# Optimization experiments

Measured on AMD Instinct MI355X. Metric: run time of the kernel, lower is better.

## Reference

```python
import jax, jax.numpy as jnp
import numpy as np

DIM = 256
HEAD_DIM = 32
HEADS = DIM // HEAD_DIM
SHAPE = (64, 64)          # (H, W) patch grid
WS = 8                    # window size
SHIFT = 4                 # shift size (ws // 2)
SCALE = HEAD_DIM ** -0.5
WS2 = WS * WS


def _rel_indices(ws):
    # relative position index for every (query, key) pair in a window
    a = np.arange(ws)
    y1, x1, y2, x2 = np.meshgrid(a, a, a, a, indexing='ij')
    idx = (y1 - y2 + ws - 1) * (2 * ws - 1) + (x1 - x2 + ws - 1)
    return idx.reshape(ws * ws, ws * ws)  # (ws2, ws2)


def _shift_mask(shape, ws, shift):
    # region labels per patch, 9 regions from the 3x3 slice grid
    H, W = shape
    region = np.zeros((H, W), dtype=np.int32)
    slices = [slice(0, -ws), slice(-ws, -shift), slice(-shift, None)]
    num = 0
    for i in slices:
        for j in slices:
            region[i, j] = num
            num += 1
    # window-partition the region map -> (n_windows, ws2)
    nH, nW = H // ws, W // ws
    r = region.reshape(nH, ws, nW, ws).transpose(0, 2, 1, 3).reshape(nH * nW, ws * ws)
    # True where query and key come from different regions
    return (r[:, None, :] - r[:, :, None]) != 0  # (nw, ws2, ws2)


REL_IDX = jnp.asarray(_rel_indices(WS))                 # (ws2, ws2) int
MASK = jnp.asarray(_shift_mask(SHAPE, WS, SHIFT))       # (nw, ws2, ws2) bool


def _split_windows(x, ws):
    # (b, H, W, C) -> (b * nH * nW, ws*ws, C)
    b, H, W, C = x.shape
    x = x.reshape(b, H // ws, ws, W // ws, ws, C)
    x = x.transpose(0, 1, 3, 2, 4, 5)
    return x.reshape(-1, ws * ws, C)


def _merge_windows(x, shape, ws):
    # inverse of _split_windows
    H, W = shape
    nH, nW = H // ws, W // ws
    C = x.shape[-1]
    x = x.reshape(-1, nH, nW, ws, ws, C)
    x = x.transpose(0, 1, 3, 2, 4, 5)
    return x.reshape(-1, H, W, C)


def setup_inputs() -> dict:
    key = jax.random.key(0)
    ks = jax.random.split(key, 6)
    s = 0.02
    return {
        'x': jax.random.normal(ks[0], (32, SHAPE[0] * SHAPE[1], DIM), jnp.float32),
        'w_qkv': jax.random.normal(ks[1], (3 * DIM, DIM), jnp.float32) * s,
        'b_qkv': jax.random.normal(ks[2], (3 * DIM,), jnp.float32) * s,
        'w_out': jax.random.normal(ks[3], (DIM, DIM), jnp.float32) * s,
        'b_out': jax.random.normal(ks[4], (DIM,), jnp.float32) * s,
        'pos_enc': jax.random.normal(ks[5], (HEADS, (2 * WS - 1) ** 2), jnp.float32) * s,
    }


def reference(x, w_qkv, b_qkv, w_out, b_out, pos_enc):
    B, N, C = x.shape
    H, W = SHAPE
    nw = (H // WS) * (W // WS)

    xg = x.reshape(B, H, W, C)
    if SHIFT > 0:
        xg = jnp.roll(xg, (-SHIFT, -SHIFT), axis=(1, 2))
    xw = _split_windows(xg, WS)                        # (B*nw, ws2, C)

    qkv = xw @ w_qkv.T + b_qkv                         # (B*nw, ws2, 3C)
    qkv = qkv.reshape(-1, WS2, 3, HEADS, HEAD_DIM)
    q, k, v = (qkv[:, :, i].transpose(0, 2, 1, 3) for i in range(3))  # (Bn, h, ws2, hd)

    attn = jnp.einsum('bhqd,bhkd->bhqk', q, k) * SCALE  # (Bn, h, ws2, ws2)
    bias = pos_enc[:, REL_IDX]                          # (h, ws2, ws2)
    attn = attn + bias[None]

    if SHIFT > 0:
        attn = attn.reshape(B, nw, HEADS, WS2, WS2)
        attn = jnp.where(MASK[None, :, None], -jnp.inf, attn)
        attn = attn.reshape(B * nw, HEADS, WS2, WS2)

    attn = jax.nn.softmax(attn, axis=-1)
    out = jnp.einsum('bhqk,bhkd->bhqd', attn, v)        # (Bn, h, ws2, hd)
    out = out.transpose(0, 2, 1, 3).reshape(-1, WS2, C)
    out = out @ w_out.T + b_out                         # (Bn, ws2, C)

    out = _merge_windows(out, SHAPE, WS)                # (B, H, W, C)
    if SHIFT > 0:
        out = jnp.roll(out, (SHIFT, SHIFT), axis=(1, 2))
    return out.reshape(B, N, C)
```

## Files before the change

kernel.cpp:

```cpp
#include <hip/hip_runtime.h>
#include <stdint.h>


typedef short short8 __attribute__((ext_vector_type(8)));
typedef short s16x4 __attribute__((ext_vector_type(4)));
typedef float f32x4 __attribute__((ext_vector_type(4)));

typedef __attribute__((address_space(1))) uint32_t g_u32;
typedef __attribute__((address_space(3))) uint32_t l_u32;

#define SCALE 0.17677669529663687f

__device__ __forceinline__ uint16_t f2bf(float f) {
  union { float f; uint32_t u; } c; c.f = f;
  uint32_t r = c.u + 0x7FFFu + ((c.u >> 16) & 1u);
  return (uint16_t)(r >> 16);
}

__device__ __forceinline__ void g2lds16(const void* g, void* l) {
  __builtin_amdgcn_global_load_lds((const g_u32*)g, (l_u32*)l, 16, 0, 0);
}

__global__ __launch_bounds__(256) void cvtw_kernel(const float* __restrict__ wq,
                                                   const float* __restrict__ wo,
                                                   uint16_t* __restrict__ out) {
  int i = (blockIdx.x * 256 + threadIdx.x) * 8;
  const float* src = (i < 196608) ? (wq + i) : (wo + (i - 196608));
  f32x4 a = *(const f32x4*)src;
  f32x4 b = *(const f32x4*)(src + 4);
  short8 v;
  v[0] = (short)f2bf(a[0]); v[1] = (short)f2bf(a[1]);
  v[2] = (short)f2bf(a[2]); v[3] = (short)f2bf(a[3]);
  v[4] = (short)f2bf(b[0]); v[5] = (short)f2bf(b[1]);
  v[6] = (short)f2bf(b[2]); v[7] = (short)f2bf(b[3]);
  *(short8*)(out + i) = v;
}

__global__ __launch_bounds__(256) void bias_kernel(const float* __restrict__ pe,
                                                   float* __restrict__ bm) {
  int bx = blockIdx.x;
  int wd = bx >> 3, head = bx & 7;
  int hw = wd >> 3, ww = wd & 7;
  int tid = threadIdx.x;
  int kk = tid >> 2, a0 = (tid & 3) * 4;
  int jy = kk >> 3, jx = kk & 7;
  int hj = hw * 8 + jy, xj = ww * 8 + jx;
  int rj = (hj >= 60 ? 2 : (hj >= 56 ? 1 : 0)) * 3 + (xj >= 60 ? 2 : (xj >= 56 ? 1 : 0));
  float* dst = bm + (size_t)bx * 4096 + kk * 64 + a0 * 4;
  for (int aa = 0; aa < 4; ++aa) {
    int a = a0 + aa;
    f32x4 v;
#pragma unroll
    for (int ni = 0; ni < 4; ++ni) {
      int i = ni * 16 + a;
      int iy = i >> 3, ix = i & 7;
      int hi = hw * 8 + iy, xi = ww * 8 + ix;
      int ri = (hi >= 60 ? 2 : (hi >= 56 ? 1 : 0)) * 3 + (xi >= 60 ? 2 : (xi >= 56 ? 1 : 0));
      v[ni] = (ri != rj) ? -1e30f : pe[head * 225 + (iy - jy + 7) * 15 + (ix - jx + 7)];
    }
    *(f32x4*)(dst + aa * 4) = v;
  }
}

__global__ __launch_bounds__(256, 2) void wattn_kernel(
    const float* __restrict__ x, const uint16_t* __restrict__ wq,
    const float* __restrict__ bqkv, const float* __restrict__ bm,
    uint16_t* __restrict__ ao) {
  __shared__ uint16_t sm[40960];
  uint16_t* As = sm;
  const int tid = threadIdx.x, lane = tid & 63, wv = tid >> 6;
  const int quad = lane >> 4, l15 = lane & 15;
  const int b = blockIdx.x;
  const int w = ((b >> 4) << 3) + (b & 7);
  const int hh = (b >> 3) & 1;
  const int h = hh * 4 + wv;
  const int wd = w & 63, bb = w >> 6;
  f32x4 zero = {0.f, 0.f, 0.f, 0.f};

  {
    const int rl = tid >> 3;
    const int cg = tid & 7;
#pragma unroll
    for (int pass = 0; pass < 2; ++pass) {
      int row = pass * 32 + rl;
      int hy = (wd >> 3) * 8 + (row >> 3);
      int xx = (wd & 7) * 8 + (row & 7);
      const float* sp = x + (size_t)(bb * 4096 + (((hy + 4) & 63) << 6) + ((xx + 4) & 63)) * 256;
      int psw = (row >> 1) & 3;
#pragma unroll
      for (int j = 0; j < 4; ++j) {
        int c0 = cg * 8 + j * 64;
        f32x4 a = *(const f32x4*)(sp + c0);
        f32x4 d = *(const f32x4*)(sp + c0 + 4);
        short8 v;
        v[0] = (short)f2bf(a[0]); v[1] = (short)f2bf(a[1]);
        v[2] = (short)f2bf(a[2]); v[3] = (short)f2bf(a[3]);
        v[4] = (short)f2bf(d[0]); v[5] = (short)f2bf(d[1]);
        v[6] = (short)f2bf(d[2]); v[7] = (short)f2bf(d[3]);
        int ks = c0 >> 5, g = (c0 >> 3) & 3;
        *(short8*)&As[(ks * 64 + row) * 32 + ((g ^ psw) << 3)] = v;
      }
    }
  }

  const int fsw = (quad ^ ((l15 >> 1) & 3)) << 3;
  uint16_t* qk = sm + 16384 + wv * 6144;

  const uint16_t* bb0 = wq + (size_t)(h * 32 + l15) * 256 + quad * 8;

  short8 bfr[2][6];
#pragma unroll
  for (int ni = 0; ni < 6; ++ni)
    bfr[0][ni] = *(const short8*)(bb0 + (ni >> 1) * 65536 + (ni & 1) * 4096);

  f32x4 acc[4][6];
#pragma unroll
  for (int mi = 0; mi < 4; ++mi)
#pragma unroll
    for (int ni = 0; ni < 6; ++ni) acc[mi][ni] = zero;

  __syncthreads();

#pragma unroll
  for (int ks = 0; ks < 8; ++ks) {
    const int cur = ks & 1;
    if (ks < 7) {
#pragma unroll
      for (int ni = 0; ni < 6; ++ni)
        bfr[cur ^ 1][ni] = *(const short8*)(bb0 + (ni >> 1) * 65536 + (ni & 1) * 4096 + (ks + 1) * 32);
    }
    short8 af[4];
#pragma unroll
    for (int mi = 0; mi < 4; ++mi)
      af[mi] = *(const short8*)&As[(ks * 64 + mi * 16 + l15) * 32 + fsw];
#pragma unroll
    for (int mi = 0; mi < 4; ++mi)
#pragma unroll
      for (int ni = 0; ni < 6; ++ni)
        acc[mi][ni] = __builtin_amdgcn_mfma_f32_16x16x32_bf16(af[mi], bfr[cur][ni], acc[mi][ni], 0, 0, 0);
  }

  float bqv[6];
#pragma unroll
  for (int ni = 0; ni < 6; ++ni)
    bqv[ni] = bqkv[(ni >> 1) * 256 + h * 32 + (ni & 1) * 16 + l15];

#pragma unroll
  for (int ni = 0; ni < 4; ++ni) {
    uint16_t* dst = qk + (ni >> 1) * 2048;
    int d = (ni & 1) * 16 + l15, dg = d >> 3;
#pragma unroll
    for (int mi = 0; mi < 4; ++mi)
#pragma unroll
      for (int r = 0; r < 4; ++r) {
        int t = mi * 16 + quad * 4 + r;
        dst[t * 32 + (((dg ^ ((t >> 1) & 3)) << 3) | (d & 7))] =
            f2bf(acc[mi][ni][r] + bqv[ni]);
      }
  }
  {
    uint16_t* vdst = qk + 4096;
#pragma unroll
    for (int ni = 4; ni < 6; ++ni) {
      int d = (ni - 4) * 16 + l15;
#pragma unroll
      for (int mi = 0; mi < 4; ++mi) {
        int t0 = mi * 16 + quad * 4;
        s16x4 pv;
        pv[0] = (short)f2bf(acc[mi][ni][0] + bqv[ni]);
        pv[1] = (short)f2bf(acc[mi][ni][1] + bqv[ni]);
        pv[2] = (short)f2bf(acc[mi][ni][2] + bqv[ni]);
        pv[3] = (short)f2bf(acc[mi][ni][3] + bqv[ni]);
        *(s16x4*)&vdst[d * 64 + (t0 ^ ((d & 7) << 3))] = pv;
      }
    }
  }

  __syncthreads();

  const uint16_t* qb2 = qk;
  const uint16_t* kb2 = qk + 2048;
  const uint16_t* vb2 = qk + 4096;
  const float* bmh = bm + ((size_t)wd * 8 + h) * 4096;

  short8 ak[4], bq[4];
#pragma unroll
  for (int mi = 0; mi < 4; ++mi)
    ak[mi] = *(const short8*)&kb2[(mi * 16 + l15) * 32 + fsw];
#pragma unroll
  for (int ni = 0; ni < 4; ++ni)
    bq[ni] = *(const short8*)&qb2[(ni * 16 + l15) * 32 + fsw];

  f32x4 s[4][4];
#pragma unroll
  for (int mi = 0; mi < 4; ++mi)
#pragma unroll
    for (int ni = 0; ni < 4; ++ni)
      s[mi][ni] = __builtin_amdgcn_mfma_f32_16x16x32_bf16(ak[mi], bq[ni], zero, 0, 0, 0);

#pragma unroll
  for (int mi = 0; mi < 4; ++mi)
#pragma unroll
    for (int r = 0; r < 4; ++r) {
      int kk = mi * 16 + quad * 4 + r;
      f32x4 b4 = *(const f32x4*)&bmh[kk * 64 + l15 * 4];
#pragma unroll
      for (int ni = 0; ni < 4; ++ni)
        s[mi][ni][r] = s[mi][ni][r] * SCALE + b4[ni];
    }

#pragma unroll
  for (int ni = 0; ni < 4; ++ni) {
    float mx = s[0][ni][0];
#pragma unroll
    for (int mi = 0; mi < 4; ++mi)
#pragma unroll
      for (int r = 0; r < 4; ++r) mx = fmaxf(mx, s[mi][ni][r]);
    mx = fmaxf(mx, __shfl_xor(mx, 16, 64));
    mx = fmaxf(mx, __shfl_xor(mx, 32, 64));
    float sum = 0.f;
#pragma unroll
    for (int mi = 0; mi < 4; ++mi)
#pragma unroll
      for (int r = 0; r < 4; ++r) {
        float e = __expf(s[mi][ni][r] - mx);
        s[mi][ni][r] = e;
        sum += e;
      }
    sum += __shfl_xor(sum, 16, 64);
    sum += __shfl_xor(sum, 32, 64);
    float inv = 1.f / sum;
#pragma unroll
    for (int mi = 0; mi < 4; ++mi)
#pragma unroll
      for (int r = 0; r < 4; ++r) s[mi][ni][r] *= inv;
  }

  uint16_t* Pw = sm + wv * 4096;
#pragma unroll
  for (int mi = 0; mi < 4; ++mi)
#pragma unroll
    for (int ni = 0; ni < 4; ++ni)
#pragma unroll
      for (int rp = 0; rp < 2; ++rp) {
        int kk = mi * 16 + quad * 4 + rp * 2;
        int q = ni * 16 + l15;
        uint32_t pk = (uint32_t)f2bf(s[mi][ni][rp * 2]) |
                      ((uint32_t)f2bf(s[mi][ni][rp * 2 + 1]) << 16);
        *(uint32_t*)&Pw[q * 64 + ((((kk >> 3) ^ (q & 7)) << 3) | (kk & 7))] = pk;
      }

  f32x4 o[4][2];
#pragma unroll
  for (int mi = 0; mi < 4; ++mi) { o[mi][0] = zero; o[mi][1] = zero; }
#pragma unroll
  for (int ki = 0; ki < 2; ++ki) {
    int tc = ki * 32 + quad * 8;
    short8 vf0 = *(const short8*)&vb2[l15 * 64 + (tc ^ ((l15 & 7) << 3))];
    short8 vf1 = *(const short8*)&vb2[(16 + l15) * 64 + (tc ^ ((l15 & 7) << 3))];
#pragma unroll
    for (int mi = 0; mi < 4; ++mi) {
      int q = mi * 16 + l15;
      short8 pa = *(const short8*)&Pw[q * 64 + (((ki * 4 + quad) ^ (q & 7)) << 3)];
      o[mi][0] = __builtin_amdgcn_mfma_f32_16x16x32_bf16(pa, vf0, o[mi][0], 0, 0, 0);
      o[mi][1] = __builtin_amdgcn_mfma_f32_16x16x32_bf16(pa, vf1, o[mi][1], 0, 0, 0);
    }
  }
#pragma unroll
  for (int mi = 0; mi < 4; ++mi)
#pragma unroll
    for (int ni = 0; ni < 2; ++ni)
#pragma unroll
      for (int r = 0; r < 4; ++r) {
        int t = mi * 16 + quad * 4 + r;
        ao[(size_t)(w * 64 + t) * 256 + h * 32 + ni * 16 + l15] = f2bf(o[mi][ni][r]);
      }
}

__global__ __launch_bounds__(256) void oproj_kernel(
    const uint16_t* __restrict__ aob, const uint16_t* __restrict__ wo,
    const float* __restrict__ bout, float* __restrict__ out) {
  __shared__ uint16_t sm[16384];
  uint16_t* As = sm;
  uint16_t* Bs = sm + 8192;
  const int tid = threadIdx.x, lane = tid & 63, wv = tid >> 6;
  const int quad = lane >> 4, l15 = lane & 15;
  const int n0 = blockIdx.x * 128;
  const int m0 = blockIdx.y * 128;

  const int c0 = wv * 2, c1 = c0 + 1;
  const int perm = ((lane & 3) ^ ((lane >> 3) & 3)) * 8;
  const int fsw = (quad ^ ((l15 >> 1) & 3)) * 8;
  const uint16_t* ap0 = aob + (size_t)(m0 + c0 * 16 + (lane >> 2)) * 256 + perm;
  const uint16_t* ap1 = aob + (size_t)(m0 + c1 * 16 + (lane >> 2)) * 256 + perm;
  const uint16_t* bp0 = wo + (size_t)(n0 + c0 * 16 + (lane >> 2)) * 256 + perm;
  const uint16_t* bp1 = wo + (size_t)(n0 + c1 * 16 + (lane >> 2)) * 256 + perm;

  const int wm = (wv & 1) * 64, wn = (wv >> 1) * 64;
  f32x4 zero = {0.f, 0.f, 0.f, 0.f};
  f32x4 acc[4][4];
#pragma unroll
  for (int mi = 0; mi < 4; ++mi)
#pragma unroll
    for (int ni = 0; ni < 4; ++ni) acc[mi][ni] = zero;

  g2lds16(ap0, &As[c0 * 512]);
  g2lds16(ap1, &As[c1 * 512]);
  g2lds16(bp0, &Bs[c0 * 512]);
  g2lds16(bp1, &Bs[c1 * 512]);

#pragma unroll
  for (int ks = 0; ks < 8; ++ks) {
    __syncthreads();
    if (ks < 7) {
      int nb = ((ks + 1) & 1) * 4096, k0 = (ks + 1) * 32;
      g2lds16(ap0 + k0, &As[nb + c0 * 512]);
      g2lds16(ap1 + k0, &As[nb + c1 * 512]);
      g2lds16(bp0 + k0, &Bs[nb + c0 * 512]);
      g2lds16(bp1 + k0, &Bs[nb + c1 * 512]);
    }
    int buf = (ks & 1) * 4096;
    short8 af[4], bf[4];
#pragma unroll
    for (int mi = 0; mi < 4; ++mi)
      af[mi] = *(const short8*)&As[buf + (wm + mi * 16 + l15) * 32 + fsw];
#pragma unroll
    for (int ni = 0; ni < 4; ++ni)
      bf[ni] = *(const short8*)&Bs[buf + (wn + ni * 16 + l15) * 32 + fsw];
#pragma unroll
    for (int mi = 0; mi < 4; ++mi)
#pragma unroll
      for (int ni = 0; ni < 4; ++ni)
        acc[mi][ni] = __builtin_amdgcn_mfma_f32_16x16x32_bf16(af[mi], bf[ni], acc[mi][ni], 0, 0, 0);
  }

  float bo4[4];
#pragma unroll
  for (int ni = 0; ni < 4; ++ni) bo4[ni] = bout[n0 + wn + ni * 16 + l15];
#pragma unroll
  for (int mi = 0; mi < 4; ++mi) {
    int mb = m0 + wm + mi * 16 + quad * 4;
    int w = mb >> 6, t0 = mb & 63;
    int b = w >> 6, wd = w & 63;
    int hw2 = wd >> 3, ww2 = wd & 7;
#pragma unroll
    for (int r = 0; r < 4; ++r) {
      int t = t0 + r;
      int h = hw2 * 8 + (t >> 3), xx = ww2 * 8 + (t & 7);
      int row = (((h + 4) & 63) << 6) | ((xx + 4) & 63);
      float* op = out + ((size_t)b * 4096 + row) * 256 + n0 + wn;
#pragma unroll
      for (int ni = 0; ni < 4; ++ni) op[ni * 16 + l15] = acc[mi][ni][r] + bo4[ni];
    }
  }
}

extern "C" void kernel_launch(void* const* d_in, const int* in_sizes, int n_in,
                              void* d_out, int out_size, void* d_ws, size_t ws_size,
                              hipStream_t stream) {
  const float* x = (const float*)d_in[0];
  const float* w_qkv = (const float*)d_in[1];
  const float* b_qkv = (const float*)d_in[2];
  const float* w_out = (const float*)d_in[3];
  const float* b_out = (const float*)d_in[4];
  const float* pos_enc = (const float*)d_in[5];
  float* out = (float*)d_out;

  uint8_t* ws = (uint8_t*)d_ws;
  uint16_t* aob = (uint16_t*)(ws);
  uint16_t* wqb = (uint16_t*)(ws + 67108864);
  uint16_t* wob = (uint16_t*)(ws + 67502080);
  float*    bmt = (float*)   (ws + 67633152);

  cvtw_kernel<<<128, 256, 0, stream>>>(w_qkv, w_out, wqb);
  bias_kernel<<<512, 256, 0, stream>>>(pos_enc, bmt);
  wattn_kernel<<<4096, 256, 0, stream>>>(x, wqb, b_qkv, bmt, aob);
  oproj_kernel<<<dim3(2, 1024), 256, 0, stream>>>(aob, wob, b_out, out);
}
```

Baseline: 367.7 us.

## Fuse output projection into window-attention kernel with one block per window

Merges the attention kernel and the separate output-projection GEMM into one kernel. Each 512-thread block now handles one window with all eight heads (one wave per head), stages the per-head attention output in LDS in bf16, and runs the output projection from LDS with weights streamed from global memory. This removes the bf16 intermediate round trip through global memory and one launch. The trade-offs are higher LDS use (128KB per block), a block-wide barrier, and a P matrix staged in two halves to fit.

```diff
diff --git a/kernel.cpp b/kernel.cpp
--- a/kernel.cpp
+++ b/kernel.cpp
@@ -5,9 +5,6 @@
 typedef short short8 __attribute__((ext_vector_type(8)));
 typedef short s16x4 __attribute__((ext_vector_type(4)));
 typedef float f32x4 __attribute__((ext_vector_type(4)));
-
-typedef __attribute__((address_space(1))) uint32_t g_u32;
-typedef __attribute__((address_space(3))) uint32_t l_u32;
 
 #define SCALE 0.17677669529663687f
 
@@ -15,10 +12,6 @@
   union { float f; uint32_t u; } c; c.f = f;
   uint32_t r = c.u + 0x7FFFu + ((c.u >> 16) & 1u);
   return (uint16_t)(r >> 16);
-}
-
-__device__ __forceinline__ void g2lds16(const void* g, void* l) {
-  __builtin_amdgcn_global_load_lds((const g_u32*)g, (l_u32*)l, 16, 0, 0);
 }
 
 __global__ __launch_bounds__(256) void cvtw_kernel(const float* __restrict__ wq,
@@ -62,44 +55,39 @@
   }
 }
 
-__global__ __launch_bounds__(256, 2) void wattn_kernel(
+__global__ __launch_bounds__(512, 2) void swattn_kernel(
     const float* __restrict__ x, const uint16_t* __restrict__ wq,
-    const float* __restrict__ bqkv, const float* __restrict__ bm,
-    uint16_t* __restrict__ ao) {
-  __shared__ uint16_t sm[40960];
+    const uint16_t* __restrict__ wo, const float* __restrict__ bqkv,
+    const float* __restrict__ bout, const float* __restrict__ bm,
+    float* __restrict__ out) {
+  __shared__ uint16_t sm[65536];
   uint16_t* As = sm;
   const int tid = threadIdx.x, lane = tid & 63, wv = tid >> 6;
   const int quad = lane >> 4, l15 = lane & 15;
-  const int b = blockIdx.x;
-  const int w = ((b >> 4) << 3) + (b & 7);
-  const int hh = (b >> 3) & 1;
-  const int h = hh * 4 + wv;
+  const int w = blockIdx.x;
+  const int h = wv;
   const int wd = w & 63, bb = w >> 6;
   f32x4 zero = {0.f, 0.f, 0.f, 0.f};
 
   {
-    const int rl = tid >> 3;
+    const int row = tid >> 3;
     const int cg = tid & 7;
-#pragma unroll
-    for (int pass = 0; pass < 2; ++pass) {
-      int row = pass * 32 + rl;
-      int hy = (wd >> 3) * 8 + (row >> 3);
-      int xx = (wd & 7) * 8 + (row & 7);
-      const float* sp = x + (size_t)(bb * 4096 + (((hy + 4) & 63) << 6) + ((xx + 4) & 63)) * 256;
-      int psw = (row >> 1) & 3;
-#pragma unroll
-      for (int j = 0; j < 4; ++j) {
-        int c0 = cg * 8 + j * 64;
-        f32x4 a = *(const f32x4*)(sp + c0);
-        f32x4 d = *(const f32x4*)(sp + c0 + 4);
-        short8 v;
-        v[0] = (short)f2bf(a[0]); v[1] = (short)f2bf(a[1]);
-        v[2] = (short)f2bf(a[2]); v[3] = (short)f2bf(a[3]);
-        v[4] = (short)f2bf(d[0]); v[5] = (short)f2bf(d[1]);
-        v[6] = (short)f2bf(d[2]); v[7] = (short)f2bf(d[3]);
-        int ks = c0 >> 5, g = (c0 >> 3) & 3;
-        *(short8*)&As[(ks * 64 + row) * 32 + ((g ^ psw) << 3)] = v;
-      }
+    int hy = (wd >> 3) * 8 + (row >> 3);
+    int xx = (wd & 7) * 8 + (row & 7);
+    const float* sp = x + (size_t)(bb * 4096 + (((hy + 4) & 63) << 6) + ((xx + 4) & 63)) * 256;
+    int psw = (row >> 1) & 3;
+#pragma unroll
+    for (int j = 0; j < 4; ++j) {
+      int c0 = cg * 8 + j * 64;
+      f32x4 a = *(const f32x4*)(sp + c0);
+      f32x4 d = *(const f32x4*)(sp + c0 + 4);
+      short8 v;
+      v[0] = (short)f2bf(a[0]); v[1] = (short)f2bf(a[1]);
+      v[2] = (short)f2bf(a[2]); v[3] = (short)f2bf(a[3]);
+      v[4] = (short)f2bf(d[0]); v[5] = (short)f2bf(d[1]);
+      v[6] = (short)f2bf(d[2]); v[7] = (short)f2bf(d[3]);
+      int ks = c0 >> 5, g = (c0 >> 3) & 3;
+      *(short8*)&As[(ks * 64 + row) * 32 + ((g ^ psw) << 3)] = v;
     }
   }
 
@@ -236,121 +224,102 @@
       for (int r = 0; r < 4; ++r) s[mi][ni][r] *= inv;
   }
 
-  uint16_t* Pw = sm + wv * 4096;
-#pragma unroll
-  for (int mi = 0; mi < 4; ++mi)
-#pragma unroll
-    for (int ni = 0; ni < 4; ++ni)
-#pragma unroll
-      for (int rp = 0; rp < 2; ++rp) {
-        int kk = mi * 16 + quad * 4 + rp * 2;
-        int q = ni * 16 + l15;
-        uint32_t pk = (uint32_t)f2bf(s[mi][ni][rp * 2]) |
-                      ((uint32_t)f2bf(s[mi][ni][rp * 2 + 1]) << 16);
-        *(uint32_t*)&Pw[q * 64 + ((((kk >> 3) ^ (q & 7)) << 3) | (kk & 7))] = pk;
-      }
-
+  uint16_t* Pw = sm + wv * 2048;
   f32x4 o[4][2];
 #pragma unroll
   for (int mi = 0; mi < 4; ++mi) { o[mi][0] = zero; o[mi][1] = zero; }
 #pragma unroll
-  for (int ki = 0; ki < 2; ++ki) {
-    int tc = ki * 32 + quad * 8;
-    short8 vf0 = *(const short8*)&vb2[l15 * 64 + (tc ^ ((l15 & 7) << 3))];
-    short8 vf1 = *(const short8*)&vb2[(16 + l15) * 64 + (tc ^ ((l15 & 7) << 3))];
-#pragma unroll
-    for (int mi = 0; mi < 4; ++mi) {
-      int q = mi * 16 + l15;
-      short8 pa = *(const short8*)&Pw[q * 64 + (((ki * 4 + quad) ^ (q & 7)) << 3)];
-      o[mi][0] = __builtin_amdgcn_mfma_f32_16x16x32_bf16(pa, vf0, o[mi][0], 0, 0, 0);
-      o[mi][1] = __builtin_amdgcn_mfma_f32_16x16x32_bf16(pa, vf1, o[mi][1], 0, 0, 0);
-    }
-  }
-#pragma unroll
-  for (int mi = 0; mi < 4; ++mi)
-#pragma unroll
-    for (int ni = 0; ni < 2; ++ni)
-#pragma unroll
-      for (int r = 0; r < 4; ++r) {
-        int t = mi * 16 + quad * 4 + r;
-        ao[(size_t)(w * 64 + t) * 256 + h * 32 + ni * 16 + l15] = f2bf(o[mi][ni][r]);
-      }
-}
-
-__global__ __launch_bounds__(256) void oproj_kernel(
-    const uint16_t* __restrict__ aob, const uint16_t* __restrict__ wo,
-    const float* __restrict__ bout, float* __restrict__ out) {
-  __shared__ uint16_t sm[16384];
-  uint16_t* As = sm;
-  uint16_t* Bs = sm + 8192;
-  const int tid = threadIdx.x, lane = tid & 63, wv = tid >> 6;
-  const int quad = lane >> 4, l15 = lane & 15;
-  const int n0 = blockIdx.x * 128;
-  const int m0 = blockIdx.y * 128;
-
-  const int c0 = wv * 2, c1 = c0 + 1;
-  const int perm = ((lane & 3) ^ ((lane >> 3) & 3)) * 8;
-  const int fsw = (quad ^ ((l15 >> 1) & 3)) * 8;
-  const uint16_t* ap0 = aob + (size_t)(m0 + c0 * 16 + (lane >> 2)) * 256 + perm;
-  const uint16_t* ap1 = aob + (size_t)(m0 + c1 * 16 + (lane >> 2)) * 256 + perm;
-  const uint16_t* bp0 = wo + (size_t)(n0 + c0 * 16 + (lane >> 2)) * 256 + perm;
-  const uint16_t* bp1 = wo + (size_t)(n0 + c1 * 16 + (lane >> 2)) * 256 + perm;
-
-  const int wm = (wv & 1) * 64, wn = (wv >> 1) * 64;
-  f32x4 zero = {0.f, 0.f, 0.f, 0.f};
-  f32x4 acc[4][4];
-#pragma unroll
-  for (int mi = 0; mi < 4; ++mi)
-#pragma unroll
-    for (int ni = 0; ni < 4; ++ni) acc[mi][ni] = zero;
-
-  g2lds16(ap0, &As[c0 * 512]);
-  g2lds16(ap1, &As[c1 * 512]);
-  g2lds16(bp0, &Bs[c0 * 512]);
-  g2lds16(bp1, &Bs[c1 * 512]);
+  for (int p = 0; p < 2; ++p) {
+#pragma unroll
+    for (int mi = 0; mi < 4; ++mi)
+#pragma unroll
+      for (int nn = 0; nn < 2; ++nn) {
+        int ni = 2 * p + nn;
+        int qp = nn * 16 + l15;
+#pragma unroll
+        for (int rp = 0; rp < 2; ++rp) {
+          int kk = mi * 16 + quad * 4 + rp * 2;
+          uint32_t pk = (uint32_t)f2bf(s[mi][ni][rp * 2]) |
+                        ((uint32_t)f2bf(s[mi][ni][rp * 2 + 1]) << 16);
+          *(uint32_t*)&Pw[qp * 64 + ((((kk >> 3) ^ (qp & 7)) << 3) | (kk & 7))] = pk;
+        }
+      }
+#pragma unroll
+    for (int ki = 0; ki < 2; ++ki) {
+      int tc = ki * 32 + quad * 8;
+      short8 vf0 = *(const short8*)&vb2[l15 * 64 + (tc ^ ((l15 & 7) << 3))];
+      short8 vf1 = *(const short8*)&vb2[(16 + l15) * 64 + (tc ^ ((l15 & 7) << 3))];
+#pragma unroll
+      for (int mi2 = 0; mi2 < 2; ++mi2) {
+        int mi = 2 * p + mi2;
+        int qp = mi2 * 16 + l15;
+        short8 pa = *(const short8*)&Pw[qp * 64 + (((ki * 4 + quad) ^ (qp & 7)) << 3)];
+        o[mi][0] = __builtin_amdgcn_mfma_f32_16x16x32_bf16(pa, vf0, o[mi][0], 0, 0, 0);
+        o[mi][1] = __builtin_amdgcn_mfma_f32_16x16x32_bf16(pa, vf1, o[mi][1], 0, 0, 0);
+      }
+    }
+  }
+
+  {
+    uint16_t* aodst = qk;
+#pragma unroll
+    for (int ni = 0; ni < 2; ++ni) {
+      int d = ni * 16 + l15, dg = d >> 3;
+#pragma unroll
+      for (int mi = 0; mi < 4; ++mi)
+#pragma unroll
+        for (int r = 0; r < 4; ++r) {
+          int t = mi * 16 + quad * 4 + r;
+          aodst[t * 32 + (((dg ^ ((t >> 1) & 3)) << 3) | (d & 7))] = f2bf(o[mi][ni][r]);
+        }
+    }
+  }
+
+  __syncthreads();
+
+  const uint16_t* bbase2 = wo + (size_t)(wv * 32 + l15) * 256 + quad * 8;
+  short8 bfr2[2][2];
+#pragma unroll
+  for (int ni = 0; ni < 2; ++ni)
+    bfr2[0][ni] = *(const short8*)(bbase2 + ni * 4096);
+
+  f32x4 acc2[4][2];
+#pragma unroll
+  for (int mi = 0; mi < 4; ++mi) { acc2[mi][0] = zero; acc2[mi][1] = zero; }
 
 #pragma unroll
   for (int ks = 0; ks < 8; ++ks) {
-    __syncthreads();
+    const int cur = ks & 1;
     if (ks < 7) {
-      int nb = ((ks + 1) & 1) * 4096, k0 = (ks + 1) * 32;
-      g2lds16(ap0 + k0, &As[nb + c0 * 512]);
-      g2lds16(ap1 + k0, &As[nb + c1 * 512]);
-      g2lds16(bp0 + k0, &Bs[nb + c0 * 512]);
-      g2lds16(bp1 + k0, &Bs[nb + c1 * 512]);
-    }
-    int buf = (ks & 1) * 4096;
-    short8 af[4], bf[4];
-#pragma unroll
-    for (int mi = 0; mi < 4; ++mi)
-      af[mi] = *(const short8*)&As[buf + (wm + mi * 16 + l15) * 32 + fsw];
-#pragma unroll
-    for (int ni = 0; ni < 4; ++ni)
-      bf[ni] = *(const short8*)&Bs[buf + (wn + ni * 16 + l15) * 32 + fsw];
-#pragma unroll
-    for (int mi = 0; mi < 4; ++mi)
-#pragma unroll
-      for (int ni = 0; ni < 4; ++ni)
-        acc[mi][ni] = __builtin_amdgcn_mfma_f32_16x16x32_bf16(af[mi], bf[ni], acc[mi][ni], 0, 0, 0);
-  }
-
-  float bo4[4];
-#pragma unroll
-  for (int ni = 0; ni < 4; ++ni) bo4[ni] = bout[n0 + wn + ni * 16 + l15];
+#pragma unroll
+      for (int ni = 0; ni < 2; ++ni)
+        bfr2[cur ^ 1][ni] = *(const short8*)(bbase2 + ni * 4096 + (ks + 1) * 32);
+    }
+    short8 af2[4];
+#pragma unroll
+    for (int mi = 0; mi < 4; ++mi)
+      af2[mi] = *(const short8*)&sm[16384 + ks * 6144 + (mi * 16 + l15) * 32 + fsw];
+#pragma unroll
+    for (int mi = 0; mi < 4; ++mi)
+#pragma unroll
+      for (int ni = 0; ni < 2; ++ni)
+        acc2[mi][ni] = __builtin_amdgcn_mfma_f32_16x16x32_bf16(af2[mi], bfr2[cur][ni], acc2[mi][ni], 0, 0, 0);
+  }
+
+  float bo4[2];
+#pragma unroll
+  for (int ni = 0; ni < 2; ++ni) bo4[ni] = bout[wv * 32 + ni * 16 + l15];
+  const int hw2 = wd >> 3, ww2 = wd & 7;
 #pragma unroll
   for (int mi = 0; mi < 4; ++mi) {
-    int mb = m0 + wm + mi * 16 + quad * 4;
-    int w = mb >> 6, t0 = mb & 63;
-    int b = w >> 6, wd = w & 63;
-    int hw2 = wd >> 3, ww2 = wd & 7;
 #pragma unroll
     for (int r = 0; r < 4; ++r) {
-      int t = t0 + r;
-      int h = hw2 * 8 + (t >> 3), xx = ww2 * 8 + (t & 7);
-      int row = (((h + 4) & 63) << 6) | ((xx + 4) & 63);
-      float* op = out + ((size_t)b * 4096 + row) * 256 + n0 + wn;
-#pragma unroll
-      for (int ni = 0; ni < 4; ++ni) op[ni * 16 + l15] = acc[mi][ni][r] + bo4[ni];
+      int t = mi * 16 + quad * 4 + r;
+      int hy = hw2 * 8 + (t >> 3), xx = ww2 * 8 + (t & 7);
+      int row = (((hy + 4) & 63) << 6) | ((xx + 4) & 63);
+      float* op = out + ((size_t)bb * 4096 + row) * 256 + wv * 32;
+#pragma unroll
+      for (int ni = 0; ni < 2; ++ni) op[ni * 16 + l15] = acc2[mi][ni][r] + bo4[ni];
     }
   }
 }
@@ -367,13 +336,11 @@
   float* out = (float*)d_out;
 
   uint8_t* ws = (uint8_t*)d_ws;
-  uint16_t* aob = (uint16_t*)(ws);
-  uint16_t* wqb = (uint16_t*)(ws + 67108864);
-  uint16_t* wob = (uint16_t*)(ws + 67502080);
-  float*    bmt = (float*)   (ws + 67633152);
+  uint16_t* wqb = (uint16_t*)(ws);
+  uint16_t* wob = (uint16_t*)(ws + 393216);
+  float*    bmt = (float*)   (ws + 524288);
 
   cvtw_kernel<<<128, 256, 0, stream>>>(w_qkv, w_out, wqb);
   bias_kernel<<<512, 256, 0, stream>>>(pos_enc, bmt);
-  wattn_kernel<<<4096, 256, 0, stream>>>(x, wqb, b_qkv, bmt, aob);
-  oproj_kernel<<<dim3(2, 1024), 256, 0, stream>>>(aob, wob, b_out, out);
-}
+  swattn_kernel<<<2048, 512, 0, stream>>>(x, wqb, wob, b_qkv, b_out, bmt, out);
+}
```

Result: slower. 407.7 us (+10.9%).

## Shrink window-attention LDS footprint to fit three blocks per CU

Applied to the files above, without the earlier changes.

Cuts the wattn kernel's shared memory from 80KB to 48KB so three blocks can share a CU, and raises the launch-bounds occupancy hint to 3. To fit, the X tile is staged in two K-halves with an extra barrier. Q is written late into the freed A region, and the softmax probabilities are written and consumed in two 32-query halves that reuse the Q buffer. The gain in latency hiding from more resident blocks is traded for extra syncs, serialized P staging, and tighter register limits that may cause spills.

```diff
diff --git a/kernel.cpp b/kernel.cpp
--- a/kernel.cpp
+++ b/kernel.cpp
@@ -62,11 +62,11 @@
   }
 }
 
-__global__ __launch_bounds__(256, 2) void wattn_kernel(
+__global__ __launch_bounds__(256, 3) void wattn_kernel(
     const float* __restrict__ x, const uint16_t* __restrict__ wq,
     const float* __restrict__ bqkv, const float* __restrict__ bm,
     uint16_t* __restrict__ ao) {
-  __shared__ uint16_t sm[40960];
+  __shared__ uint16_t sm[24576];
   uint16_t* As = sm;
   const int tid = threadIdx.x, lane = tid & 63, wv = tid >> 6;
   const int quad = lane >> 4, l15 = lane & 15;
@@ -77,37 +77,16 @@
   const int wd = w & 63, bb = w >> 6;
   f32x4 zero = {0.f, 0.f, 0.f, 0.f};
 
+  const int srow = tid >> 2, scg = tid & 3;
+  const float* sp;
   {
-    const int rl = tid >> 3;
-    const int cg = tid & 7;
-#pragma unroll
-    for (int pass = 0; pass < 2; ++pass) {
-      int row = pass * 32 + rl;
-      int hy = (wd >> 3) * 8 + (row >> 3);
-      int xx = (wd & 7) * 8 + (row & 7);
-      const float* sp = x + (size_t)(bb * 4096 + (((hy + 4) & 63) << 6) + ((xx + 4) & 63)) * 256;
-      int psw = (row >> 1) & 3;
-#pragma unroll
-      for (int j = 0; j < 4; ++j) {
-        int c0 = cg * 8 + j * 64;
-        f32x4 a = *(const f32x4*)(sp + c0);
-        f32x4 d = *(const f32x4*)(sp + c0 + 4);
-        short8 v;
-        v[0] = (short)f2bf(a[0]); v[1] = (short)f2bf(a[1]);
-        v[2] = (short)f2bf(a[2]); v[3] = (short)f2bf(a[3]);
-        v[4] = (short)f2bf(d[0]); v[5] = (short)f2bf(d[1]);
-        v[6] = (short)f2bf(d[2]); v[7] = (short)f2bf(d[3]);
-        int ks = c0 >> 5, g = (c0 >> 3) & 3;
-        *(short8*)&As[(ks * 64 + row) * 32 + ((g ^ psw) << 3)] = v;
-      }
-    }
-  }
-
-  const int fsw = (quad ^ ((l15 >> 1) & 3)) << 3;
-  uint16_t* qk = sm + 16384 + wv * 6144;
+    int hy = (wd >> 3) * 8 + (srow >> 3);
+    int xx = (wd & 7) * 8 + (srow & 7);
+    sp = x + (size_t)(bb * 4096 + (((hy + 4) & 63) << 6) + ((xx + 4) & 63)) * 256;
+  }
+  const int spsw = (srow >> 1) & 3;
 
   const uint16_t* bb0 = wq + (size_t)(h * 32 + l15) * 256 + quad * 8;
-
   short8 bfr[2][6];
 #pragma unroll
   for (int ni = 0; ni < 6; ++ni)
@@ -119,47 +98,63 @@
 #pragma unroll
     for (int ni = 0; ni < 6; ++ni) acc[mi][ni] = zero;
 
-  __syncthreads();
-
-#pragma unroll
-  for (int ks = 0; ks < 8; ++ks) {
-    const int cur = ks & 1;
-    if (ks < 7) {
-#pragma unroll
-      for (int ni = 0; ni < 6; ++ni)
-        bfr[cur ^ 1][ni] = *(const short8*)(bb0 + (ni >> 1) * 65536 + (ni & 1) * 4096 + (ks + 1) * 32);
-    }
-    short8 af[4];
-#pragma unroll
-    for (int mi = 0; mi < 4; ++mi)
-      af[mi] = *(const short8*)&As[(ks * 64 + mi * 16 + l15) * 32 + fsw];
-#pragma unroll
-    for (int mi = 0; mi < 4; ++mi)
-#pragma unroll
-      for (int ni = 0; ni < 6; ++ni)
-        acc[mi][ni] = __builtin_amdgcn_mfma_f32_16x16x32_bf16(af[mi], bfr[cur][ni], acc[mi][ni], 0, 0, 0);
-  }
-
+  const int fsw = (quad ^ ((l15 >> 1) & 3)) << 3;
+
+  for (int hf = 0; hf < 2; ++hf) {
+    if (hf) __syncthreads();
+#pragma unroll
+    for (int j = 0; j < 4; ++j) {
+      int c0 = scg * 8 + j * 32;
+      const float* p = sp + hf * 128 + c0;
+      f32x4 a = *(const f32x4*)p;
+      f32x4 d = *(const f32x4*)(p + 4);
+      short8 v;
+      v[0] = (short)f2bf(a[0]); v[1] = (short)f2bf(a[1]);
+      v[2] = (short)f2bf(a[2]); v[3] = (short)f2bf(a[3]);
+      v[4] = (short)f2bf(d[0]); v[5] = (short)f2bf(d[1]);
+      v[6] = (short)f2bf(d[2]); v[7] = (short)f2bf(d[3]);
+      *(short8*)&As[(j * 64 + srow) * 32 + ((scg ^ spsw) << 3)] = v;
+    }
+    __syncthreads();
+#pragma unroll
+    for (int ksl = 0; ksl < 4; ++ksl) {
+      const int ks = hf * 4 + ksl;
+      const int cur = ks & 1;
+      if (ks < 7) {
+#pragma unroll
+        for (int ni = 0; ni < 6; ++ni)
+          bfr[cur ^ 1][ni] = *(const short8*)(bb0 + (ni >> 1) * 65536 + (ni & 1) * 4096 + (ks + 1) * 32);
+      }
+      short8 af[4];
+#pragma unroll
+      for (int mi = 0; mi < 4; ++mi)
+        af[mi] = *(const short8*)&As[(ksl * 64 + mi * 16 + l15) * 32 + fsw];
+#pragma unroll
+      for (int mi = 0; mi < 4; ++mi)
+#pragma unroll
+        for (int ni = 0; ni < 6; ++ni)
+          acc[mi][ni] = __builtin_amdgcn_mfma_f32_16x16x32_bf16(af[mi], bfr[cur][ni], acc[mi][ni], 0, 0, 0);
+    }
+  }
+
+  uint16_t* kvs = sm + 8192 + wv * 4096;
   float bqv[6];
 #pragma unroll
   for (int ni = 0; ni < 6; ++ni)
     bqv[ni] = bqkv[(ni >> 1) * 256 + h * 32 + (ni & 1) * 16 + l15];
 
 #pragma unroll
-  for (int ni = 0; ni < 4; ++ni) {
-    uint16_t* dst = qk + (ni >> 1) * 2048;
-    int d = (ni & 1) * 16 + l15, dg = d >> 3;
-#pragma unroll
-    for (int mi = 0; mi < 4; ++mi)
-#pragma unroll
-      for (int r = 0; r < 4; ++r) {
-        int t = mi * 16 + quad * 4 + r;
-        dst[t * 32 + (((dg ^ ((t >> 1) & 3)) << 3) | (d & 7))] =
-            f2bf(acc[mi][ni][r] + bqv[ni]);
-      }
+  for (int ni = 2; ni < 4; ++ni) {
+    int d = (ni & 1) * 16 + l15;
+    uint16_t* kd = kvs + quad * 4 * 32 + ((((d >> 3) ^ quad) << 3) | (d & 7));
+#pragma unroll
+    for (int mi = 0; mi < 4; ++mi)
+#pragma unroll
+      for (int r = 0; r < 4; ++r)
+        kd[mi * 512 + r * 32] = f2bf(acc[mi][ni][r] + bqv[ni]);
   }
   {
-    uint16_t* vdst = qk + 4096;
+    uint16_t* vdst = kvs + 2048;
 #pragma unroll
     for (int ni = 4; ni < 6; ++ni) {
       int d = (ni - 4) * 16 + l15;
@@ -178,19 +173,28 @@
 
   __syncthreads();
 
-  const uint16_t* qb2 = qk;
-  const uint16_t* kb2 = qk + 2048;
-  const uint16_t* vb2 = qk + 4096;
+  uint16_t* sq = sm + wv * 2048;
+#pragma unroll
+  for (int ni = 0; ni < 2; ++ni) {
+    int d = ni * 16 + l15;
+    uint16_t* qd = sq + quad * 4 * 32 + ((((d >> 3) ^ quad) << 3) | (d & 7));
+#pragma unroll
+    for (int mi = 0; mi < 4; ++mi)
+#pragma unroll
+      for (int r = 0; r < 4; ++r)
+        qd[mi * 512 + r * 32] = f2bf(acc[mi][ni][r] + bqv[ni]);
+  }
+
+  const int fsw2 = (quad ^ ((l15 >> 2) & 3)) << 3;
+  short8 bq[4], ak[4];
+#pragma unroll
+  for (int ni = 0; ni < 4; ++ni)
+    bq[ni] = *(const short8*)&sq[(ni * 16 + l15) * 32 + fsw2];
+#pragma unroll
+  for (int mi = 0; mi < 4; ++mi)
+    ak[mi] = *(const short8*)&kvs[(mi * 16 + l15) * 32 + fsw2];
+
   const float* bmh = bm + ((size_t)wd * 8 + h) * 4096;
-
-  short8 ak[4], bq[4];
-#pragma unroll
-  for (int mi = 0; mi < 4; ++mi)
-    ak[mi] = *(const short8*)&kb2[(mi * 16 + l15) * 32 + fsw];
-#pragma unroll
-  for (int ni = 0; ni < 4; ++ni)
-    bq[ni] = *(const short8*)&qb2[(ni * 16 + l15) * 32 + fsw];
-
   f32x4 s[4][4];
 #pragma unroll
   for (int mi = 0; mi < 4; ++mi)
@@ -236,36 +240,43 @@
       for (int r = 0; r < 4; ++r) s[mi][ni][r] *= inv;
   }
 
-  uint16_t* Pw = sm + wv * 4096;
-#pragma unroll
-  for (int mi = 0; mi < 4; ++mi)
-#pragma unroll
-    for (int ni = 0; ni < 4; ++ni)
-#pragma unroll
-      for (int rp = 0; rp < 2; ++rp) {
-        int kk = mi * 16 + quad * 4 + rp * 2;
-        int q = ni * 16 + l15;
-        uint32_t pk = (uint32_t)f2bf(s[mi][ni][rp * 2]) |
-                      ((uint32_t)f2bf(s[mi][ni][rp * 2 + 1]) << 16);
-        *(uint32_t*)&Pw[q * 64 + ((((kk >> 3) ^ (q & 7)) << 3) | (kk & 7))] = pk;
-      }
-
+  uint16_t* Pw = sq;
+  const uint16_t* vb2 = kvs + 2048;
   f32x4 o[4][2];
 #pragma unroll
   for (int mi = 0; mi < 4; ++mi) { o[mi][0] = zero; o[mi][1] = zero; }
 #pragma unroll
-  for (int ki = 0; ki < 2; ++ki) {
-    int tc = ki * 32 + quad * 8;
-    short8 vf0 = *(const short8*)&vb2[l15 * 64 + (tc ^ ((l15 & 7) << 3))];
-    short8 vf1 = *(const short8*)&vb2[(16 + l15) * 64 + (tc ^ ((l15 & 7) << 3))];
-#pragma unroll
-    for (int mi = 0; mi < 4; ++mi) {
-      int q = mi * 16 + l15;
-      short8 pa = *(const short8*)&Pw[q * 64 + (((ki * 4 + quad) ^ (q & 7)) << 3)];
-      o[mi][0] = __builtin_amdgcn_mfma_f32_16x16x32_bf16(pa, vf0, o[mi][0], 0, 0, 0);
-      o[mi][1] = __builtin_amdgcn_mfma_f32_16x16x32_bf16(pa, vf1, o[mi][1], 0, 0, 0);
-    }
-  }
+  for (int p = 0; p < 2; ++p) {
+#pragma unroll
+    for (int mi = 0; mi < 4; ++mi)
+#pragma unroll
+      for (int nn = 0; nn < 2; ++nn) {
+        int ni = 2 * p + nn;
+        int qp = nn * 16 + l15;
+#pragma unroll
+        for (int rp = 0; rp < 2; ++rp) {
+          int kk = mi * 16 + quad * 4 + rp * 2;
+          uint32_t pk = (uint32_t)f2bf(s[mi][ni][rp * 2]) |
+                        ((uint32_t)f2bf(s[mi][ni][rp * 2 + 1]) << 16);
+          *(uint32_t*)&Pw[qp * 64 + ((((kk >> 3) ^ (qp & 7)) << 3) | (kk & 7))] = pk;
+        }
+      }
+#pragma unroll
+    for (int ki = 0; ki < 2; ++ki) {
+      int tc = ki * 32 + quad * 8;
+      short8 vf0 = *(const short8*)&vb2[l15 * 64 + (tc ^ ((l15 & 7) << 3))];
+      short8 vf1 = *(const short8*)&vb2[(16 + l15) * 64 + (tc ^ ((l15 & 7) << 3))];
+#pragma unroll
+      for (int mi2 = 0; mi2 < 2; ++mi2) {
+        int mi = 2 * p + mi2;
+        int qp = mi2 * 16 + l15;
+        short8 pa = *(const short8*)&Pw[qp * 64 + (((ki * 4 + quad) ^ (qp & 7)) << 3)];
+        o[mi][0] = __builtin_amdgcn_mfma_f32_16x16x32_bf16(pa, vf0, o[mi][0], 0, 0, 0);
+        o[mi][1] = __builtin_amdgcn_mfma_f32_16x16x32_bf16(pa, vf1, o[mi][1], 0, 0, 0);
+      }
+    }
+  }
+
 #pragma unroll
   for (int mi = 0; mi < 4; ++mi)
 #pragma unroll
```

Result: no change. 371.1 us (+0.9%).

## Process all heads of a window per 512-thread block with aliased LDS buffers

Applied to the files above, without the earlier changes.

The window-attention kernel now launches one 512-thread block per window, with each of 8 waves handling one head. Previously two 256-thread blocks each took 4 heads, so each window's input tile was loaded from global memory and converted to bf16 twice; now it is done once. LDS use drops from 80 KB to 64 KB by reusing one per-wave region for Q, then K, then the probability matrix, which is written and consumed in two halves, with V kept separately. The smaller footprint aims to fit more resident waves per CU. The cost is tighter ordering of LDS reuse inside each wave and larger blocks.

```diff
diff --git a/kernel.cpp b/kernel.cpp
--- a/kernel.cpp
+++ b/kernel.cpp
@@ -62,52 +62,44 @@
   }
 }
 
-__global__ __launch_bounds__(256, 2) void wattn_kernel(
+__global__ __launch_bounds__(512, 4) void wattn_kernel(
     const float* __restrict__ x, const uint16_t* __restrict__ wq,
     const float* __restrict__ bqkv, const float* __restrict__ bm,
     uint16_t* __restrict__ ao) {
-  __shared__ uint16_t sm[40960];
+  __shared__ uint16_t sm[32768];
   uint16_t* As = sm;
   const int tid = threadIdx.x, lane = tid & 63, wv = tid >> 6;
   const int quad = lane >> 4, l15 = lane & 15;
-  const int b = blockIdx.x;
-  const int w = ((b >> 4) << 3) + (b & 7);
-  const int hh = (b >> 3) & 1;
-  const int h = hh * 4 + wv;
+  const int w = blockIdx.x;
+  const int h = wv;
   const int wd = w & 63, bb = w >> 6;
   f32x4 zero = {0.f, 0.f, 0.f, 0.f};
 
   {
-    const int rl = tid >> 3;
+    const int row = tid >> 3;
     const int cg = tid & 7;
-#pragma unroll
-    for (int pass = 0; pass < 2; ++pass) {
-      int row = pass * 32 + rl;
-      int hy = (wd >> 3) * 8 + (row >> 3);
-      int xx = (wd & 7) * 8 + (row & 7);
-      const float* sp = x + (size_t)(bb * 4096 + (((hy + 4) & 63) << 6) + ((xx + 4) & 63)) * 256;
-      int psw = (row >> 1) & 3;
-#pragma unroll
-      for (int j = 0; j < 4; ++j) {
-        int c0 = cg * 8 + j * 64;
-        f32x4 a = *(const f32x4*)(sp + c0);
-        f32x4 d = *(const f32x4*)(sp + c0 + 4);
-        short8 v;
-        v[0] = (short)f2bf(a[0]); v[1] = (short)f2bf(a[1]);
-        v[2] = (short)f2bf(a[2]); v[3] = (short)f2bf(a[3]);
-        v[4] = (short)f2bf(d[0]); v[5] = (short)f2bf(d[1]);
-        v[6] = (short)f2bf(d[2]); v[7] = (short)f2bf(d[3]);
-        int ks = c0 >> 5, g = (c0 >> 3) & 3;
-        *(short8*)&As[(ks * 64 + row) * 32 + ((g ^ psw) << 3)] = v;
-      }
+    int hy = (wd >> 3) * 8 + (row >> 3);
+    int xx = (wd & 7) * 8 + (row & 7);
+    const float* sp = x + (size_t)(bb * 4096 + (((hy + 4) & 63) << 6) + ((xx + 4) & 63)) * 256;
+    int psw = (row >> 1) & 3;
+#pragma unroll
+    for (int j = 0; j < 4; ++j) {
+      int c0 = cg * 8 + j * 64;
+      f32x4 a = *(const f32x4*)(sp + c0);
+      f32x4 d = *(const f32x4*)(sp + c0 + 4);
+      short8 v;
+      v[0] = (short)f2bf(a[0]); v[1] = (short)f2bf(a[1]);
+      v[2] = (short)f2bf(a[2]); v[3] = (short)f2bf(a[3]);
+      v[4] = (short)f2bf(d[0]); v[5] = (short)f2bf(d[1]);
+      v[6] = (short)f2bf(d[2]); v[7] = (short)f2bf(d[3]);
+      int ks = c0 >> 5, g = (c0 >> 3) & 3;
+      *(short8*)&As[(ks * 64 + row) * 32 + ((g ^ psw) << 3)] = v;
     }
   }
 
   const int fsw = (quad ^ ((l15 >> 1) & 3)) << 3;
-  uint16_t* qk = sm + 16384 + wv * 6144;
 
   const uint16_t* bb0 = wq + (size_t)(h * 32 + l15) * 256 + quad * 8;
-
   short8 bfr[2][6];
 #pragma unroll
   for (int ni = 0; ni < 6; ++ni)
@@ -145,52 +137,61 @@
   for (int ni = 0; ni < 6; ++ni)
     bqv[ni] = bqkv[(ni >> 1) * 256 + h * 32 + (ni & 1) * 16 + l15];
 
-#pragma unroll
-  for (int ni = 0; ni < 4; ++ni) {
-    uint16_t* dst = qk + (ni >> 1) * 2048;
-    int d = (ni & 1) * 16 + l15, dg = d >> 3;
+  uint16_t* vdst = sm + 16384 + wv * 2048;
+#pragma unroll
+  for (int ni = 4; ni < 6; ++ni) {
+    int d = (ni - 4) * 16 + l15;
+#pragma unroll
+    for (int mi = 0; mi < 4; ++mi) {
+      int t0 = mi * 16 + quad * 4;
+      s16x4 pv;
+      pv[0] = (short)f2bf(acc[mi][ni][0] + bqv[ni]);
+      pv[1] = (short)f2bf(acc[mi][ni][1] + bqv[ni]);
+      pv[2] = (short)f2bf(acc[mi][ni][2] + bqv[ni]);
+      pv[3] = (short)f2bf(acc[mi][ni][3] + bqv[ni]);
+      *(s16x4*)&vdst[d * 64 + (t0 ^ ((d & 7) << 3))] = pv;
+    }
+  }
+
+  __syncthreads();
+
+  uint16_t* S = sm + wv * 2048;
+
+#pragma unroll
+  for (int ni = 0; ni < 2; ++ni) {
+    int d = ni * 16 + l15, dg = d >> 3;
 #pragma unroll
     for (int mi = 0; mi < 4; ++mi)
 #pragma unroll
       for (int r = 0; r < 4; ++r) {
         int t = mi * 16 + quad * 4 + r;
-        dst[t * 32 + (((dg ^ ((t >> 1) & 3)) << 3) | (d & 7))] =
+        S[t * 32 + (((dg ^ ((t >> 1) & 3)) << 3) | (d & 7))] =
             f2bf(acc[mi][ni][r] + bqv[ni]);
       }
   }
-  {
-    uint16_t* vdst = qk + 4096;
-#pragma unroll
-    for (int ni = 4; ni < 6; ++ni) {
-      int d = (ni - 4) * 16 + l15;
-#pragma unroll
-      for (int mi = 0; mi < 4; ++mi) {
-        int t0 = mi * 16 + quad * 4;
-        s16x4 pv;
-        pv[0] = (short)f2bf(acc[mi][ni][0] + bqv[ni]);
-        pv[1] = (short)f2bf(acc[mi][ni][1] + bqv[ni]);
-        pv[2] = (short)f2bf(acc[mi][ni][2] + bqv[ni]);
-        pv[3] = (short)f2bf(acc[mi][ni][3] + bqv[ni]);
-        *(s16x4*)&vdst[d * 64 + (t0 ^ ((d & 7) << 3))] = pv;
-      }
-    }
-  }
-
-  __syncthreads();
-
-  const uint16_t* qb2 = qk;
-  const uint16_t* kb2 = qk + 2048;
-  const uint16_t* vb2 = qk + 4096;
+  short8 bq[4];
+#pragma unroll
+  for (int ni = 0; ni < 4; ++ni)
+    bq[ni] = *(const short8*)&S[(ni * 16 + l15) * 32 + fsw];
+
+#pragma unroll
+  for (int ni = 2; ni < 4; ++ni) {
+    int d = (ni & 1) * 16 + l15, dg = d >> 3;
+#pragma unroll
+    for (int mi = 0; mi < 4; ++mi)
+#pragma unroll
+      for (int r = 0; r < 4; ++r) {
+        int t = mi * 16 + quad * 4 + r;
+        S[t * 32 + (((dg ^ ((t >> 1) & 3)) << 3) | (d & 7))] =
+            f2bf(acc[mi][ni][r] + bqv[ni]);
+      }
+  }
+  short8 ak[4];
+#pragma unroll
+  for (int mi = 0; mi < 4; ++mi)
+    ak[mi] = *(const short8*)&S[(mi * 16 + l15) * 32 + fsw];
+
   const float* bmh = bm + ((size_t)wd * 8 + h) * 4096;
-
-  short8 ak[4], bq[4];
-#pragma unroll
-  for (int mi = 0; mi < 4; ++mi)
-    ak[mi] = *(const short8*)&kb2[(mi * 16 + l15) * 32 + fsw];
-#pragma unroll
-  for (int ni = 0; ni < 4; ++ni)
-    bq[ni] = *(const short8*)&qb2[(ni * 16 + l15) * 32 + fsw];
-
   f32x4 s[4][4];
 #pragma unroll
   for (int mi = 0; mi < 4; ++mi)
@@ -236,36 +237,43 @@
       for (int r = 0; r < 4; ++r) s[mi][ni][r] *= inv;
   }
 
-  uint16_t* Pw = sm + wv * 4096;
-#pragma unroll
-  for (int mi = 0; mi < 4; ++mi)
-#pragma unroll
-    for (int ni = 0; ni < 4; ++ni)
-#pragma unroll
-      for (int rp = 0; rp < 2; ++rp) {
-        int kk = mi * 16 + quad * 4 + rp * 2;
-        int q = ni * 16 + l15;
-        uint32_t pk = (uint32_t)f2bf(s[mi][ni][rp * 2]) |
-                      ((uint32_t)f2bf(s[mi][ni][rp * 2 + 1]) << 16);
-        *(uint32_t*)&Pw[q * 64 + ((((kk >> 3) ^ (q & 7)) << 3) | (kk & 7))] = pk;
-      }
-
+  uint16_t* Pw = S;
+  const uint16_t* vb2 = vdst;
   f32x4 o[4][2];
 #pragma unroll
   for (int mi = 0; mi < 4; ++mi) { o[mi][0] = zero; o[mi][1] = zero; }
 #pragma unroll
-  for (int ki = 0; ki < 2; ++ki) {
-    int tc = ki * 32 + quad * 8;
-    short8 vf0 = *(const short8*)&vb2[l15 * 64 + (tc ^ ((l15 & 7) << 3))];
-    short8 vf1 = *(const short8*)&vb2[(16 + l15) * 64 + (tc ^ ((l15 & 7) << 3))];
-#pragma unroll
-    for (int mi = 0; mi < 4; ++mi) {
-      int q = mi * 16 + l15;
-      short8 pa = *(const short8*)&Pw[q * 64 + (((ki * 4 + quad) ^ (q & 7)) << 3)];
-      o[mi][0] = __builtin_amdgcn_mfma_f32_16x16x32_bf16(pa, vf0, o[mi][0], 0, 0, 0);
-      o[mi][1] = __builtin_amdgcn_mfma_f32_16x16x32_bf16(pa, vf1, o[mi][1], 0, 0, 0);
-    }
-  }
+  for (int p = 0; p < 2; ++p) {
+#pragma unroll
+    for (int mi = 0; mi < 4; ++mi)
+#pragma unroll
+      for (int nn = 0; nn < 2; ++nn) {
+        int ni = 2 * p + nn;
+        int qp = nn * 16 + l15;
+#pragma unroll
+        for (int rp = 0; rp < 2; ++rp) {
+          int kk = mi * 16 + quad * 4 + rp * 2;
+          uint32_t pk = (uint32_t)f2bf(s[mi][ni][rp * 2]) |
+                        ((uint32_t)f2bf(s[mi][ni][rp * 2 + 1]) << 16);
+          *(uint32_t*)&Pw[qp * 64 + ((((kk >> 3) ^ (qp & 7)) << 3) | (kk & 7))] = pk;
+        }
+      }
+#pragma unroll
+    for (int ki = 0; ki < 2; ++ki) {
+      int tc = ki * 32 + quad * 8;
+      short8 vf0 = *(const short8*)&vb2[l15 * 64 + (tc ^ ((l15 & 7) << 3))];
+      short8 vf1 = *(const short8*)&vb2[(16 + l15) * 64 + (tc ^ ((l15 & 7) << 3))];
+#pragma unroll
+      for (int mi2 = 0; mi2 < 2; ++mi2) {
+        int mi = 2 * p + mi2;
+        int qp = mi2 * 16 + l15;
+        short8 pa = *(const short8*)&Pw[qp * 64 + (((ki * 4 + quad) ^ (qp & 7)) << 3)];
+        o[mi][0] = __builtin_amdgcn_mfma_f32_16x16x32_bf16(pa, vf0, o[mi][0], 0, 0, 0);
+        o[mi][1] = __builtin_amdgcn_mfma_f32_16x16x32_bf16(pa, vf1, o[mi][1], 0, 0, 0);
+      }
+    }
+  }
+
 #pragma unroll
   for (int mi = 0; mi < 4; ++mi)
 #pragma unroll
@@ -374,6 +382,6 @@
 
   cvtw_kernel<<<128, 256, 0, stream>>>(w_qkv, w_out, wqb);
   bias_kernel<<<512, 256, 0, stream>>>(pos_enc, bmt);
-  wattn_kernel<<<4096, 256, 0, stream>>>(x, wqb, b_qkv, bmt, aob);
+  wattn_kernel<<<2048, 512, 0, stream>>>(x, wqb, b_qkv, bmt, aob);
   oproj_kernel<<<dim3(2, 1024), 256, 0, stream>>>(aob, wob, b_out, out);
 }
```

Measured after the change: 540.4 us. 47.0% more time.
